# Kernel optimization log

Hardware: AMD Instinct MI355X
Metric: run time of the kernel (lower is better)

Reference implementation:

```python
import jax, jax.numpy as jnp
import numpy as np

B, T, C, H = 4, 1024, 2048, 16
HD = C // H          # head dim = 128 (even, as RoPE requires)
BLOCK = 1024         # config.block_size == config.max_block_size
NEG = -1e30          # finite stand-in for -inf in the additive attention bias


def setup_inputs() -> dict:
    key = jax.random.key(0)
    k1, k2, k3, k4, k5 = jax.random.split(key, 5)
    x = jax.random.normal(k1, (B, T, C), jnp.float32)
    cumulative_scores = jax.random.uniform(k2, (B, T), jnp.float32)  # kept small: fed to exp()
    token_index = jax.random.randint(k3, (B, T), 0, BLOCK, dtype=jnp.int32)
    padding_mask = jnp.ones((B, T), jnp.int32)
    # xavier-ish scale so softmax doesn't saturate
    W_attn = jax.random.normal(k4, (C, 3 * C), jnp.float32) / np.sqrt(C)
    W_proj = jax.random.normal(k5, (C, C), jnp.float32) / np.sqrt(C)
    return dict(x=x, cumulative_scores=cumulative_scores, token_index=token_index,
                padding_mask=padding_mask, W_attn=W_attn, W_proj=W_proj)


def _rotate_half(a):
    a1, a2 = a[..., : HD // 2], a[..., HD // 2:]
    return jnp.concatenate([-a2, a1], axis=-1)


def reference(x, cumulative_scores, token_index, padding_mask, W_attn, W_proj):
    # QKV projection (bias=False per config)
    qkv = x @ W_attn                                  # (B,T,3C)
    q, k, v = jnp.split(qkv, 3, axis=2)
    heads = lambda a: a.reshape(B, T, H, HD).transpose(0, 2, 1, 3)  # (B,H,T,HD)
    q, k, v = heads(q), heads(k), heads(v)

    # input-dependent partial rotation positions (exact replica of the original
    # scatter: token_index (B,T) fancy-indexes the last axis of a (B,BLOCK)
    # buffer, so counts are summed over ALL batch rows, as in the source)
    counts = jnp.zeros((B, BLOCK), jnp.float32).at[..., token_index].add(1.0)
    t = jnp.cumsum(jnp.take_along_axis(1.0 / (counts + 1e-10), token_index, axis=-1), axis=-1)  # (B,T)

    # RoPE with per-token positions t (seq_dim=-2, offset 0 for both q and k)
    inv_freq = 1.0 / (10000.0 ** (jnp.arange(0, HD, 2, dtype=jnp.float32) / HD))
    freqs = jnp.einsum('bt,j->btj', t, inv_freq)
    emb = jnp.concatenate([freqs, freqs], axis=-1)[:, None, :, :]   # (B,1,T,HD)
    sin, cos = jnp.sin(emb), jnp.cos(emb)
    q = q * cos + _rotate_half(q) * sin
    k = k * cos + _rotate_half(k) * sin

    # 'fork' plan overrides on the last rotary channel
    q = q.at[..., -1].set(1.0)
    k = k.at[..., -1].set(jnp.broadcast_to(cumulative_scores[:, None, :], (B, H, T)))

    # V rescaled by exp(cumulative_scores)
    v = v * jnp.exp(cumulative_scores)[:, None, :, None]

    # causal + key-padding additive bias, SDPA with scale 1/sqrt(HD)
    keep = jnp.tril(jnp.ones((T, T), bool))[None, None] & padding_mask.astype(bool)[:, None, None, :]
    scores = jnp.einsum('bhqd,bhkd->bhqk', q, k) / np.sqrt(HD)
    scores = jnp.where(keep, scores, NEG)
    attn = jax.nn.softmax(scores, axis=-1)
    y = jnp.einsum('bhqk,bhkd->bhqd', attn, v)

    y = y.transpose(0, 2, 1, 3).reshape(B, T, C)
    return y @ W_proj
```

## Files before the change

### kernel.cpp

```cpp
#include <hip/hip_runtime.h>

#define BB 4
#define TT 1024
#define CCH 2048
#define HH 16
#define HDIM 128
#define NBLK 1024
#define MM (BB*TT)
#define N1 (3*CCH)
#define NQT 16

typedef _Float16 f16;
typedef _Float16 half8 __attribute__((ext_vector_type(8)));
typedef _Float16 half4 __attribute__((ext_vector_type(4)));
typedef float floatx4 __attribute__((ext_vector_type(4)));

__device__ __forceinline__ void g2lds16(const void* g, void* l) {
    __builtin_amdgcn_global_load_lds((const __attribute__((address_space(1))) void*)g,
                                     (__attribute__((address_space(3))) void*)l, 16, 0, 0);
}

__global__ void k_cvt(const float* __restrict__ in, f16* __restrict__ out, int n4) {
    int i = blockIdx.x * blockDim.x + threadIdx.x;
    if (i >= n4) return;
    float4 v = ((const float4*)in)[i];
    union { ushort4 u; f16 h[4]; } o;
    o.h[0] = (f16)v.x; o.h[1] = (f16)v.y; o.h[2] = (f16)v.z; o.h[3] = (f16)v.w;
    ((ushort4*)out)[i] = o.u;
}

__global__ void k_tr(const float* __restrict__ in, f16* __restrict__ out, int R, int Cc) {
    __shared__ float tile[32][33];
    int c0 = blockIdx.x * 32, r0 = blockIdx.y * 32;
    int tx = threadIdx.x, ty = threadIdx.y;
#pragma unroll
    for (int k = 0; k < 4; k++) {
        int r = ty + k * 8;
        tile[r][tx] = in[(size_t)(r0 + r) * Cc + c0 + tx];
    }
    __syncthreads();
#pragma unroll
    for (int k = 0; k < 4; k++) {
        int r = ty + k * 8;
        out[(size_t)(c0 + r) * R + r0 + tx] = (f16)tile[tx][r];
    }
}

__global__ void k_trv(const f16* __restrict__ in, f16* __restrict__ out) {
    __shared__ f16 tile[32][34];
    int bh = blockIdx.z;
    int h0 = blockIdx.x * 32, t0 = blockIdx.y * 32;
    int tx = threadIdx.x, ty = threadIdx.y;
#pragma unroll
    for (int k = 0; k < 4; k++) {
        int t = ty + k * 8;
        tile[t][tx] = in[((size_t)bh * TT + t0 + t) * HDIM + h0 + tx];
    }
    __syncthreads();
#pragma unroll
    for (int k = 0; k < 4; k++) {
        int r = ty + k * 8;
        out[((size_t)bh * HDIM + h0 + r) * TT + t0 + tx] = tile[tx][r];
    }
}

__global__ void k_hist(const int* __restrict__ tok, int* __restrict__ cnt) {
    int i = blockIdx.x * blockDim.x + threadIdx.x;
    if (i < MM) atomicAdd(cnt + tok[i], 1);
}

__global__ __launch_bounds__(1024) void k_scan(const int* __restrict__ tok,
                                               const int* __restrict__ cnt,
                                               const int* __restrict__ pm,
                                               float* __restrict__ tpos,
                                               float* __restrict__ pb) {
    __shared__ float s[TT];
    int b = blockIdx.x, t = threadIdx.x;
    s[t] = 1.0f / ((float)cnt[tok[b * TT + t]] + 1e-10f);
    __syncthreads();
    for (int off = 1; off < TT; off <<= 1) {
        float add = (t >= off) ? s[t - off] : 0.0f;
        __syncthreads();
        s[t] += add;
        __syncthreads();
    }
    tpos[b * TT + t] = s[t];
    pb[b * TT + t] = pm[b * TT + t] ? 0.0f : -1e30f;
}

template <int MODE>
__global__ __launch_bounds__(256) void k_gemm(const f16* __restrict__ A,
                                              const f16* __restrict__ Bt,
                                              void* __restrict__ Cp,
                                              const float* __restrict__ tpos,
                                              const float* __restrict__ cs,
                                              f16* __restrict__ qr,
                                              f16* __restrict__ kr,
                                              f16* __restrict__ vsc,
                                              int Mdim, int Ndim, int Kdim) {
    const float SCALE = 0.08838834764831845f;
    __shared__ __align__(16) f16 As[128 * 32];
    __shared__ __align__(16) f16 Bs[128 * 32];
    int nbn = Ndim >> 7;
    int bm = blockIdx.x / nbn, bn = blockIdx.x % nbn;
    int tid = threadIdx.x;
    int w = tid >> 6, lane = tid & 63, quad = lane >> 4, l16 = lane & 15;
    const f16* Ab = A + (size_t)(bm << 7) * Kdim;
    const f16* Bb = Bt + (size_t)(bn << 7) * Kdim;
    int rsub = lane >> 2;
    int csub = (lane & 3) << 3;
    floatx4 acc[2][8];
#pragma unroll
    for (int i = 0; i < 2; i++)
#pragma unroll
        for (int j = 0; j < 8; j++) acc[i][j] = (floatx4){0.f, 0.f, 0.f, 0.f};
    int nk = Kdim >> 5;
    for (int kt = 0; kt < nk; kt++) {
        __syncthreads();
#pragma unroll
        for (int i = 0; i < 2; i++) {
            int row = w * 32 + i * 16 + rsub;
            g2lds16(Ab + (size_t)row * Kdim + (kt << 5) + csub, &As[(w * 32 + i * 16) * 32]);
            g2lds16(Bb + (size_t)row * Kdim + (kt << 5) + csub, &Bs[(w * 32 + i * 16) * 32]);
        }
        __syncthreads();
        half8 af[2], bfr[8];
#pragma unroll
        for (int i = 0; i < 2; i++) af[i] = *(const half8*)&As[(w * 32 + i * 16 + l16) * 32 + (quad << 3)];
#pragma unroll
        for (int j = 0; j < 8; j++) bfr[j] = *(const half8*)&Bs[(j * 16 + l16) * 32 + (quad << 3)];
#pragma unroll
        for (int i = 0; i < 2; i++)
#pragma unroll
            for (int j = 0; j < 8; j++)
                acc[i][j] = __builtin_amdgcn_mfma_f32_16x16x32_f16(af[i], bfr[j], acc[i][j], 0, 0, 0);
    }
    int row0 = (bm << 7) + w * 32 + (quad << 2);
    if (MODE == 0) {
        int cb = (bn << 7) + l16;
#pragma unroll
        for (int i = 0; i < 2; i++)
#pragma unroll
            for (int j = 0; j < 8; j++)
#pragma unroll
                for (int r = 0; r < 4; r++)
                    ((float*)Cp)[(size_t)(row0 + i * 16 + r) * Ndim + cb + j * 16] = acc[i][j][r];
    } else {
        int type = bn >> 4;
        int h = bn & 15;
        if (type < 2) {
            f16* outp = (type == 0) ? qr : kr;
            float invf[4];
#pragma unroll
            for (int jc = 0; jc < 4; jc++)
                invf[jc] = expf((float)(jc * 16 + l16) * -0.14391156929f);
#pragma unroll
            for (int i = 0; i < 2; i++)
#pragma unroll
                for (int r = 0; r < 4; r++) {
                    int row = row0 + i * 16 + r;
                    float tp = tpos[row], csv = cs[row];
                    size_t ob = ((size_t)((row >> 10) * HH + h) * TT + (row & 1023)) * HDIM + l16;
#pragma unroll
                    for (int jc = 0; jc < 4; jc++) {
                        float a1 = acc[i][jc][r], a2 = acc[i][jc + 4][r];
                        float sn, cn;
                        sincosf(tp * invf[jc], &sn, &cn);
                        float o1 = a1 * cn - a2 * sn, o2 = a2 * cn + a1 * sn;
                        if (type == 0) {
                            if (jc == 3 && l16 == 15) o2 = 1.0f;
                            o1 *= SCALE; o2 *= SCALE;
                        } else {
                            if (jc == 3 && l16 == 15) o2 = csv;
                        }
                        outp[ob + jc * 16]      = (f16)o1;
                        outp[ob + jc * 16 + 64] = (f16)o2;
                    }
                }
        } else {
#pragma unroll
            for (int i = 0; i < 2; i++)
#pragma unroll
                for (int r = 0; r < 4; r++) {
                    int row = row0 + i * 16 + r;
                    float ve = expf(cs[row]);
                    size_t ob = ((size_t)((row >> 10) * HH + h) * TT + (row & 1023)) * HDIM + l16;
#pragma unroll
                    for (int jc = 0; jc < 8; jc++)
                        vsc[ob + jc * 16] = (f16)(acc[i][jc][r] * ve);
                }
        }
    }
}

__global__ __launch_bounds__(256) void k_attn(const f16* __restrict__ qr,
                                              const f16* __restrict__ kr,
                                              const f16* __restrict__ vt,
                                              const float* __restrict__ pb,
                                              f16* __restrict__ y) {
    __shared__ __align__(16) f16 Ks[64 * 136];
    __shared__ __align__(16) f16 Vs[128 * 72];
    __shared__ float pbs[64];
    int p = blockIdx.x & (NQT / 2 - 1);
    int bh = blockIdx.x >> 3;
    int b = bh >> 4, h = bh & 15;
    int tid = threadIdx.x;
    int w = tid >> 6, lane = tid & 63, quad = lane >> 4, l16 = lane & 15;
#pragma unroll
    for (int pass = 0; pass < 2; pass++) {
        int qt = pass ? (NQT - 1 - p) : p;
        int q0 = qt << 6;
        int qg = q0 + w * 16 + l16;
        const f16* Qp = qr + ((size_t)bh * TT + qg) * HDIM;
        half8 qf[4];
#pragma unroll
        for (int kc = 0; kc < 4; kc++) qf[kc] = *(const half8*)&Qp[kc * 32 + (quad << 3)];
        floatx4 O[8];
#pragma unroll
        for (int i = 0; i < 8; i++) O[i] = (floatx4){0.f, 0.f, 0.f, 0.f};
        float mx = -1e30f, ls = 0.f;
        for (int kt = 0; kt <= qt; kt++) {
            __syncthreads();
            const f16* Kb = kr + ((size_t)bh * TT + (kt << 6)) * HDIM;
            const f16* Vb = vt + (size_t)bh * HDIM * TT + (kt << 6);
#pragma unroll
            for (int i = 0; i < 4; i++) {
                int seg = tid + (i << 8);
                int krow = seg >> 4, kcol = (seg & 15) << 3;
                *(uint4*)&Ks[krow * 136 + kcol] = *(const uint4*)&Kb[(size_t)krow * HDIM + kcol];
                int vrow = seg >> 3, vcol = (seg & 7) << 3;
                *(uint4*)&Vs[vrow * 72 + vcol] = *(const uint4*)&Vb[(size_t)vrow * TT + vcol];
            }
            if (tid < 64) pbs[tid] = pb[b * TT + (kt << 6) + tid];
            __syncthreads();
            floatx4 Sv[4];
#pragma unroll
            for (int mc = 0; mc < 4; mc++) Sv[mc] = (floatx4){0.f, 0.f, 0.f, 0.f};
#pragma unroll
            for (int kc = 0; kc < 4; kc++)
#pragma unroll
                for (int mc = 0; mc < 4; mc++) {
                    half8 kf = *(const half8*)&Ks[(mc * 16 + l16) * 136 + kc * 32 + (quad << 3)];
                    Sv[mc] = __builtin_amdgcn_mfma_f32_16x16x32_f16(kf, qf[kc], Sv[mc], 0, 0, 0);
                }
            float pv[4][4];
            float mnew = mx;
#pragma unroll
            for (int mc = 0; mc < 4; mc++) {
                float4 pbv = *(const float4*)&pbs[mc * 16 + (quad << 2)];
#pragma unroll
                for (int i = 0; i < 4; i++) {
                    int kv = (kt << 6) + mc * 16 + (quad << 2) + i;
                    float s = (kv <= qg) ? Sv[mc][i] + ((const float*)&pbv)[i] : -1e30f;
                    pv[mc][i] = s;
                    mnew = fmaxf(mnew, s);
                }
            }
            mnew = fmaxf(mnew, __shfl_xor(mnew, 16));
            mnew = fmaxf(mnew, __shfl_xor(mnew, 32));
            float al = __expf(mx - mnew);
            mx = mnew;
            float psum = 0.f;
#pragma unroll
            for (int mc = 0; mc < 4; mc++)
#pragma unroll
                for (int i = 0; i < 4; i++) {
                    float e = __expf(pv[mc][i] - mnew);
                    pv[mc][i] = e;
                    psum += e;
                }
            psum += __shfl_xor(psum, 16);
            psum += __shfl_xor(psum, 32);
            ls = ls * al + psum;
#pragma unroll
            for (int hm = 0; hm < 8; hm++)
#pragma unroll
                for (int i = 0; i < 4; i++) O[hm][i] *= al;
            half4 pf[4];
#pragma unroll
            for (int mc = 0; mc < 4; mc++) {
                pf[mc][0] = (f16)pv[mc][0]; pf[mc][1] = (f16)pv[mc][1];
                pf[mc][2] = (f16)pv[mc][2]; pf[mc][3] = (f16)pv[mc][3];
            }
#pragma unroll
            for (int mc = 0; mc < 4; mc++)
#pragma unroll
                for (int hm = 0; hm < 8; hm++) {
                    half4 vf = *(const half4*)&Vs[(hm * 16 + l16) * 72 + mc * 16 + (quad << 2)];
                    O[hm] = __builtin_amdgcn_mfma_f32_16x16x16f16(vf, pf[mc], O[hm], 0, 0, 0);
                }
        }
        float inv = 1.0f / ls;
#pragma unroll
        for (int hm = 0; hm < 8; hm++) {
            half4 ov;
#pragma unroll
            for (int i = 0; i < 4; i++) ov[i] = (f16)(O[hm][i] * inv);
            *(half4*)&y[((size_t)b * TT + qg) * CCH + h * HDIM + hm * 16 + (quad << 2)] = ov;
        }
        __syncthreads();
    }
}

extern "C" void kernel_launch(void* const* d_in, const int* in_sizes, int n_in,
                              void* d_out, int out_size, void* d_ws, size_t ws_size,
                              hipStream_t stream) {
    const float* x   = (const float*)d_in[0];
    const float* cs  = (const float*)d_in[1];
    const int*   tok = (const int*)d_in[2];
    const int*   pm  = (const int*)d_in[3];
    const float* Wa  = (const float*)d_in[4];
    const float* Wp  = (const float*)d_in[5];
    float* out = (float*)d_out;
    char* ws = (char*)d_ws;

    f16* x16 = (f16*)(ws + 0);
    f16* WaT = (f16*)(ws + 16777216);
    f16* vt  = (f16*)(ws + 41943040);
    f16* qr  = (f16*)(ws + 92274688);
    f16* kr  = (f16*)(ws + 109051904);
    f16* vsc = (f16*)(ws + 125829120);
    int*   cnt  = (int*)(ws + 142606336);
    float* tpos = (float*)(ws + 142610432);
    float* pb   = (float*)(ws + 142626816);
    f16* y   = x16;
    f16* WpT = WaT;

    hipMemsetAsync(cnt, 0, NBLK * sizeof(int), stream);
    k_hist<<<MM / 256, 256, 0, stream>>>(tok, cnt);
    k_scan<<<BB, TT, 0, stream>>>(tok, cnt, pm, tpos, pb);
    k_cvt<<<(MM * CCH / 4) / 256, 256, 0, stream>>>(x, x16, MM * CCH / 4);
    k_tr<<<dim3(N1 / 32, CCH / 32), dim3(32, 8), 0, stream>>>(Wa, WaT, CCH, N1);
    k_gemm<1><<<(MM / 128) * (N1 / 128), 256, 0, stream>>>(x16, WaT, nullptr, tpos, cs,
                                                           qr, kr, vsc, MM, N1, CCH);
    k_trv<<<dim3(4, 32, BB * HH), dim3(32, 8), 0, stream>>>(vsc, vt);
    k_tr<<<dim3(CCH / 32, CCH / 32), dim3(32, 8), 0, stream>>>(Wp, WpT, CCH, CCH);
    k_attn<<<BB * HH * (NQT / 2), 256, 0, stream>>>(qr, kr, vt, pb, y);
    k_gemm<0><<<(MM / 128) * (CCH / 128), 256, 0, stream>>>(y, WpT, out, nullptr, nullptr,
                                                            nullptr, nullptr, nullptr, MM, CCH, CCH);
}
```

Baseline: 429.8 us.

## Use 2x2 wave tiling in GEMM and fuse prep conversions into one launch

The GEMM warp layout changes from each wave owning 32 rows by 128 columns to a 2x2 grid of 64x64 wave tiles. Each k-step then needs 8 fragment loads from LDS instead of 10. Because the RoPE rotation pairs no longer sit in the same thread, the QK epilogue stages the f16 tile through shared memory to read the partner column. The x conversion and both weight transposes are merged into a single 3D-grid prep kernel, with WpT moved to its own buffer, which removes two launches and lets the work run concurrently. The trade-offs are extra LDS traffic and syncs in the epilogue, and the partner value being rounded to f16 before rotation.

After: 1.184 ms. +175.5%, slower.

```diff
diff --git a/kernel.cpp b/kernel.cpp
--- a/kernel.cpp
+++ b/kernel.cpp
@@ -20,16 +20,24 @@
                                      (__attribute__((address_space(3))) void*)l, 16, 0, 0);
 }
 
-__global__ void k_cvt(const float* __restrict__ in, f16* __restrict__ out, int n4) {
-    int i = blockIdx.x * blockDim.x + threadIdx.x;
-    if (i >= n4) return;
-    float4 v = ((const float4*)in)[i];
-    union { ushort4 u; f16 h[4]; } o;
-    o.h[0] = (f16)v.x; o.h[1] = (f16)v.y; o.h[2] = (f16)v.z; o.h[3] = (f16)v.w;
-    ((ushort4*)out)[i] = o.u;
-}
-
-__global__ void k_tr(const float* __restrict__ in, f16* __restrict__ out, int R, int Cc) {
+__global__ void k_prep(const float* __restrict__ Wa, const float* __restrict__ Wp,
+                       const float* __restrict__ x,
+                       f16* __restrict__ WaT, f16* __restrict__ WpT,
+                       f16* __restrict__ x16) {
+    int z = blockIdx.z;
+    if (z == 2) {
+        int i = (blockIdx.y * 192 + blockIdx.x) * 256 + threadIdx.x + threadIdx.y * 32;
+        if (i >= MM * CCH / 4) return;
+        float4 v = ((const float4*)x)[i];
+        union { ushort4 u; f16 h[4]; } o;
+        o.h[0] = (f16)v.x; o.h[1] = (f16)v.y; o.h[2] = (f16)v.z; o.h[3] = (f16)v.w;
+        ((ushort4*)x16)[i] = o.u;
+        return;
+    }
+    const float* in = (z == 0) ? Wa : Wp;
+    f16* out = (z == 0) ? WaT : WpT;
+    int Cc = (z == 0) ? N1 : CCH;
+    if (blockIdx.x * 32 >= Cc) return;
     __shared__ float tile[32][33];
     int c0 = blockIdx.x * 32, r0 = blockIdx.y * 32;
     int tx = threadIdx.x, ty = threadIdx.y;
@@ -42,7 +50,7 @@
 #pragma unroll
     for (int k = 0; k < 4; k++) {
         int r = ty + k * 8;
-        out[(size_t)(c0 + r) * R + r0 + tx] = (f16)tile[tx][r];
+        out[(size_t)(c0 + r) * CCH + r0 + tx] = (f16)tile[tx][r];
     }
 }
 
@@ -99,95 +107,114 @@
                                               f16* __restrict__ vsc,
                                               int Mdim, int Ndim, int Kdim) {
     const float SCALE = 0.08838834764831845f;
-    __shared__ __align__(16) f16 As[128 * 32];
-    __shared__ __align__(16) f16 Bs[128 * 32];
+    __shared__ __align__(16) f16 smem[128 * 128];
+    f16* As = smem;
+    f16* Bs = smem + 128 * 32;
     int nbn = Ndim >> 7;
     int bm = blockIdx.x / nbn, bn = blockIdx.x % nbn;
     int tid = threadIdx.x;
     int w = tid >> 6, lane = tid & 63, quad = lane >> 4, l16 = lane & 15;
-    const f16* Ab = A + (size_t)(bm << 7) * Kdim;
-    const f16* Bb = Bt + (size_t)(bn << 7) * Kdim;
+    int wm = (w & 1) << 6, wn = (w >> 1) << 6;
     int rsub = lane >> 2;
     int csub = (lane & 3) << 3;
-    floatx4 acc[2][8];
-#pragma unroll
-    for (int i = 0; i < 2; i++)
-#pragma unroll
-        for (int j = 0; j < 8; j++) acc[i][j] = (floatx4){0.f, 0.f, 0.f, 0.f};
+    const f16* pa0 = A  + (size_t)((bm << 7) + w * 32 + rsub) * Kdim + csub;
+    const f16* pa1 = pa0 + (size_t)16 * Kdim;
+    const f16* pb0 = Bt + (size_t)((bn << 7) + w * 32 + rsub) * Kdim + csub;
+    const f16* pb1 = pb0 + (size_t)16 * Kdim;
+    f16* lda0 = &As[(w * 32) * 32];
+    f16* lda1 = &As[(w * 32 + 16) * 32];
+    f16* ldb0 = &Bs[(w * 32) * 32];
+    f16* ldb1 = &Bs[(w * 32 + 16) * 32];
+    floatx4 acc[4][4];
+#pragma unroll
+    for (int i = 0; i < 4; i++)
+#pragma unroll
+        for (int j = 0; j < 4; j++) acc[i][j] = (floatx4){0.f, 0.f, 0.f, 0.f};
     int nk = Kdim >> 5;
     for (int kt = 0; kt < nk; kt++) {
         __syncthreads();
-#pragma unroll
-        for (int i = 0; i < 2; i++) {
-            int row = w * 32 + i * 16 + rsub;
-            g2lds16(Ab + (size_t)row * Kdim + (kt << 5) + csub, &As[(w * 32 + i * 16) * 32]);
-            g2lds16(Bb + (size_t)row * Kdim + (kt << 5) + csub, &Bs[(w * 32 + i * 16) * 32]);
-        }
-        __syncthreads();
-        half8 af[2], bfr[8];
-#pragma unroll
-        for (int i = 0; i < 2; i++) af[i] = *(const half8*)&As[(w * 32 + i * 16 + l16) * 32 + (quad << 3)];
-#pragma unroll
-        for (int j = 0; j < 8; j++) bfr[j] = *(const half8*)&Bs[(j * 16 + l16) * 32 + (quad << 3)];
-#pragma unroll
-        for (int i = 0; i < 2; i++)
-#pragma unroll
-            for (int j = 0; j < 8; j++)
+        g2lds16(pa0, lda0); g2lds16(pa1, lda1);
+        g2lds16(pb0, ldb0); g2lds16(pb1, ldb1);
+        pa0 += 32; pa1 += 32; pb0 += 32; pb1 += 32;
+        __syncthreads();
+        half8 af[4], bfr[4];
+#pragma unroll
+        for (int i = 0; i < 4; i++) af[i] = *(const half8*)&As[(wm + i * 16 + l16) * 32 + (quad << 3)];
+#pragma unroll
+        for (int j = 0; j < 4; j++) bfr[j] = *(const half8*)&Bs[(wn + j * 16 + l16) * 32 + (quad << 3)];
+#pragma unroll
+        for (int i = 0; i < 4; i++)
+#pragma unroll
+            for (int j = 0; j < 4; j++)
                 acc[i][j] = __builtin_amdgcn_mfma_f32_16x16x32_f16(af[i], bfr[j], acc[i][j], 0, 0, 0);
     }
-    int row0 = (bm << 7) + w * 32 + (quad << 2);
+    int rl0 = wm + (quad << 2);
+    int cl0 = wn + l16;
     if (MODE == 0) {
-        int cb = (bn << 7) + l16;
-#pragma unroll
-        for (int i = 0; i < 2; i++)
-#pragma unroll
-            for (int j = 0; j < 8; j++)
+        int rb = (bm << 7) + rl0;
+        int cb = (bn << 7) + cl0;
+#pragma unroll
+        for (int i = 0; i < 4; i++)
+#pragma unroll
+            for (int j = 0; j < 4; j++)
 #pragma unroll
                 for (int r = 0; r < 4; r++)
-                    ((float*)Cp)[(size_t)(row0 + i * 16 + r) * Ndim + cb + j * 16] = acc[i][j][r];
+                    ((float*)Cp)[(size_t)(rb + i * 16 + r) * Ndim + cb + j * 16] = acc[i][j][r];
     } else {
         int type = bn >> 4;
         int h = bn & 15;
-        if (type < 2) {
+        if (type == 2) {
+#pragma unroll
+            for (int i = 0; i < 4; i++)
+#pragma unroll
+                for (int r = 0; r < 4; r++) {
+                    int row = (bm << 7) + rl0 + i * 16 + r;
+                    float ve = expf(cs[row]);
+                    size_t ob = ((size_t)((row >> 10) * HH + h) * TT + (row & 1023)) * HDIM + cl0;
+#pragma unroll
+                    for (int j = 0; j < 4; j++)
+                        vsc[ob + j * 16] = (f16)(acc[i][j][r] * ve);
+                }
+        } else {
+            __syncthreads();
+#pragma unroll
+            for (int i = 0; i < 4; i++)
+#pragma unroll
+                for (int j = 0; j < 4; j++)
+#pragma unroll
+                    for (int r = 0; r < 4; r++)
+                        smem[(rl0 + i * 16 + r) * 128 + cl0 + j * 16] = (f16)acc[i][j][r];
+            __syncthreads();
             f16* outp = (type == 0) ? qr : kr;
             float invf[4];
 #pragma unroll
-            for (int jc = 0; jc < 4; jc++)
-                invf[jc] = expf((float)(jc * 16 + l16) * -0.14391156929f);
-#pragma unroll
-            for (int i = 0; i < 2; i++)
+            for (int j = 0; j < 4; j++)
+                invf[j] = expf((float)(((cl0 + j * 16) & 63)) * -0.14391156929f);
+#pragma unroll
+            for (int i = 0; i < 4; i++)
 #pragma unroll
                 for (int r = 0; r < 4; r++) {
-                    int row = row0 + i * 16 + r;
+                    int rloc = rl0 + i * 16 + r;
+                    int row = (bm << 7) + rloc;
                     float tp = tpos[row], csv = cs[row];
-                    size_t ob = ((size_t)((row >> 10) * HH + h) * TT + (row & 1023)) * HDIM + l16;
-#pragma unroll
-                    for (int jc = 0; jc < 4; jc++) {
-                        float a1 = acc[i][jc][r], a2 = acc[i][jc + 4][r];
+                    size_t ob = ((size_t)((row >> 10) * HH + h) * TT + (row & 1023)) * HDIM + cl0;
+#pragma unroll
+                    for (int j = 0; j < 4; j++) {
+                        int col = cl0 + j * 16;
+                        float own = acc[i][j][r];
+                        float par = (float)smem[rloc * 128 + (col ^ 64)];
                         float sn, cn;
-                        sincosf(tp * invf[jc], &sn, &cn);
-                        float o1 = a1 * cn - a2 * sn, o2 = a2 * cn + a1 * sn;
+                        sincosf(tp * invf[j], &sn, &cn);
+                        float o = (col < 64) ? (own * cn - par * sn)
+                                             : (own * cn + par * sn);
                         if (type == 0) {
-                            if (jc == 3 && l16 == 15) o2 = 1.0f;
-                            o1 *= SCALE; o2 *= SCALE;
+                            if (col == 127) o = 1.0f;
+                            o *= SCALE;
                         } else {
-                            if (jc == 3 && l16 == 15) o2 = csv;
+                            if (col == 127) o = csv;
                         }
-                        outp[ob + jc * 16]      = (f16)o1;
-                        outp[ob + jc * 16 + 64] = (f16)o2;
+                        outp[ob + j * 16] = (f16)o;
                     }
-                }
-        } else {
-#pragma unroll
-            for (int i = 0; i < 2; i++)
-#pragma unroll
-                for (int r = 0; r < 4; r++) {
-                    int row = row0 + i * 16 + r;
-                    float ve = expf(cs[row]);
-                    size_t ob = ((size_t)((row >> 10) * HH + h) * TT + (row & 1023)) * HDIM + l16;
-#pragma unroll
-                    for (int jc = 0; jc < 8; jc++)
-                        vsc[ob + jc * 16] = (f16)(acc[i][jc][r] * ve);
                 }
         }
     }
@@ -317,6 +344,7 @@
     f16* x16 = (f16*)(ws + 0);
     f16* WaT = (f16*)(ws + 16777216);
     f16* vt  = (f16*)(ws + 41943040);
+    f16* WpT = (f16*)(ws + 58720256);
     f16* qr  = (f16*)(ws + 92274688);
     f16* kr  = (f16*)(ws + 109051904);
     f16* vsc = (f16*)(ws + 125829120);
@@ -324,17 +352,14 @@
     float* tpos = (float*)(ws + 142610432);
     float* pb   = (float*)(ws + 142626816);
     f16* y   = x16;
-    f16* WpT = WaT;
 
     hipMemsetAsync(cnt, 0, NBLK * sizeof(int), stream);
     k_hist<<<MM / 256, 256, 0, stream>>>(tok, cnt);
     k_scan<<<BB, TT, 0, stream>>>(tok, cnt, pm, tpos, pb);
-    k_cvt<<<(MM * CCH / 4) / 256, 256, 0, stream>>>(x, x16, MM * CCH / 4);
-    k_tr<<<dim3(N1 / 32, CCH / 32), dim3(32, 8), 0, stream>>>(Wa, WaT, CCH, N1);
+    k_prep<<<dim3(N1 / 32, CCH / 32, 3), dim3(32, 8), 0, stream>>>(Wa, Wp, x, WaT, WpT, x16);
     k_gemm<1><<<(MM / 128) * (N1 / 128), 256, 0, stream>>>(x16, WaT, nullptr, tpos, cs,
                                                            qr, kr, vsc, MM, N1, CCH);
     k_trv<<<dim3(4, 32, BB * HH), dim3(32, 8), 0, stream>>>(vsc, vt);
-    k_tr<<<dim3(CCH / 32, CCH / 32), dim3(32, 8), 0, stream>>>(Wp, WpT, CCH, CCH);
     k_attn<<<BB * HH * (NQT / 2), 256, 0, stream>>>(qr, kr, vt, pb, y);
     k_gemm<0><<<(MM / 128) * (CCH / 128), 256, 0, stream>>>(y, WpT, out, nullptr, nullptr,
                                                             nullptr, nullptr, nullptr, MM, CCH, CCH);
```
